# Optimization experiments

Measured on AMD Instinct MI355X. Metric: run time of the kernel, lower is better.

## Reference

```python
import jax, jax.numpy as jnp
import numpy as np

N = 100000
E = 1600000
F_IN = 64
F_OUT = 64
C = 1.0
MIN_NORM = 1e-15
BALL_EPS = 4e-3  # float32 eps in HGCN PoincareBall.proj


def _norm(x):
    return jnp.clip(jnp.linalg.norm(x, axis=-1, keepdims=True), MIN_NORM)


def artanh(x):
    return jnp.arctanh(jnp.clip(x, -1.0 + 1e-7, 1.0 - 1e-7))


def proj(x, c):
    # project back onto the Poincare ball of curvature -c
    norm = _norm(x)
    maxnorm = (1.0 - BALL_EPS) / jnp.sqrt(c)
    return jnp.where(norm > maxnorm, x / norm * maxnorm, x)


def mobius_matvec(m, x, c):
    sqrt_c = jnp.sqrt(c)
    x_norm = _norm(x)
    mx = x @ m.T
    mx_norm = _norm(mx)
    res = jnp.tanh(mx_norm / x_norm * artanh(sqrt_c * x_norm)) * mx / (mx_norm * sqrt_c)
    zero_mx = jnp.all(mx == 0, axis=-1, keepdims=True)
    return jnp.where(zero_mx, jnp.zeros_like(res), res)


def expmap0(u, c):
    sqrt_c = jnp.sqrt(c)
    u_norm = _norm(u)
    return jnp.tanh(sqrt_c * u_norm) * u / (sqrt_c * u_norm)


def mobius_add(x, y, c):
    x2 = jnp.sum(x * x, axis=-1, keepdims=True)
    y2 = jnp.sum(y * y, axis=-1, keepdims=True)
    xy = jnp.sum(x * y, axis=-1, keepdims=True)
    num = (1.0 + 2.0 * c * xy + c * y2) * x + (1.0 - c * x2) * y
    denom = 1.0 + 2.0 * c * xy + c * c * x2 * y2
    return num / jnp.clip(denom, MIN_NORM)


def hyp_linear(x, W, b, c):
    res = proj(mobius_matvec(W, x, c), c)
    if b is not None:
        hyp_bias = proj(expmap0(b[None, :], c), c)
        res = proj(mobius_add(res, hyp_bias, c), c)
    return res


def scatter_mean(edge_index, x, n):
    # mean of source features over edges landing at each target node; 0 if isolated
    src, dst = edge_index[0], edge_index[1]
    s = jax.ops.segment_sum(x[src], dst, num_segments=n)
    cnt = jax.ops.segment_sum(jnp.ones((src.shape[0], 1), x.dtype), dst, num_segments=n)
    return s / jnp.clip(cnt, 1.0)


def setup_inputs() -> dict:
    key = jax.random.key(0)
    ks = jax.random.split(key, 9)
    glorot = 1.0 / np.sqrt(F_IN)
    return {
        "x": jax.random.normal(ks[0], (N, F_IN), dtype=jnp.float32) * 0.1,
        "W_pos": jax.random.uniform(ks[1], (F_OUT, F_IN), jnp.float32, -glorot, glorot),
        "W_pos_cc": jax.random.uniform(ks[2], (F_OUT, F_IN), jnp.float32, -glorot, glorot),
        "b_pos_cc": jax.random.uniform(ks[3], (F_OUT,), jnp.float32, -glorot, glorot),
        "W_neg": jax.random.uniform(ks[4], (F_OUT, F_IN), jnp.float32, -glorot, glorot),
        "W_neg_cc": jax.random.uniform(ks[5], (F_OUT, F_IN), jnp.float32, -glorot, glorot),
        "b_neg_cc": jax.random.uniform(ks[6], (F_OUT,), jnp.float32, -glorot, glorot),
        "pos_edge_index": jax.random.randint(ks[7], (2, E), 0, N, dtype=jnp.int64) if jax.config.jax_enable_x64 else jax.random.randint(ks[7], (2, E), 0, N, dtype=jnp.int32),
        "neg_edge_index": jax.random.randint(ks[8], (2, E), 0, N, dtype=jnp.int32),
    }


def reference(x, W_pos, W_pos_cc, b_pos_cc, W_neg, W_neg_cc, b_neg_cc, pos_edge_index, neg_edge_index):
    n = x.shape[0]
    # first_aggr=True branch of HSignedConv.forward
    agg_pos = scatter_mean(pos_edge_index, x, n)          # [N, F_IN]
    out_pos = hyp_linear(agg_pos, W_pos, None, C)
    out_pos = out_pos + hyp_linear(x, W_pos_cc, b_pos_cc, C)
    agg_neg = scatter_mean(neg_edge_index, x, n)
    out_neg = hyp_linear(agg_neg, W_neg, None, C)
    out_neg = out_neg + hyp_linear(x, W_neg_cc, b_neg_cc, C)
    return jnp.concatenate([out_pos, out_neg], axis=-1)  # [N, 2*F_OUT]
```

## Files before the change

### kernel.cpp

```cpp
#include <hip/hip_runtime.h>
#include <math.h>

#define NN 100000
#define BSZ 256
#define NB 391
#define NB2 782
constexpr float MAXNORM_C = 0.996f;
constexpr float MINNORM_C = 1e-15f;

__global__ void prep_transpose(const float* __restrict__ Wp, const float* __restrict__ Wpc,
                               const float* __restrict__ Wn, const float* __restrict__ Wnc,
                               float* __restrict__ wt) {
    int idx = blockIdx.x * 256 + threadIdx.x;
    int m = idx >> 12;
    int k = (idx >> 6) & 63;
    int j = idx & 63;
    const float* W = (m == 0) ? Wp : (m == 1) ? Wpc : (m == 2) ? Wn : Wnc;
    wt[idx] = W[j * 64 + k];
}

__device__ inline float wave_sum64(float v) {
    #pragma unroll
    for (int m = 32; m >= 1; m >>= 1) v += __shfl_xor(v, m, 64);
    return v;
}

__global__ void prep_bias(const float* __restrict__ bp, const float* __restrict__ bn,
                          float* __restrict__ hb) {
    int l = threadIdx.x;
    #pragma unroll
    for (int h = 0; h < 2; ++h) {
        float u = (h ? bn : bp)[l];
        float norm = fmaxf(sqrtf(wave_sum64(u * u)), MINNORM_C);
        float s = tanhf(norm) / norm;
        float v = s * u;
        float vn = fmaxf(sqrtf(wave_sum64(v * v)), MINNORM_C);
        if (vn > MAXNORM_C) v *= MAXNORM_C / vn;
        float y2 = wave_sum64(v * v);
        hb[h * 65 + l] = v;
        if (l == 0) hb[h * 65 + 64] = y2;
    }
}

__global__ __launch_bounds__(256) void bucket_count(
    const int* __restrict__ pei, int E1,
    const int* __restrict__ nei, int E2,
    int* __restrict__ gcnt) {
    __shared__ int h[NB2];
    int tid = threadIdx.x;
    for (int i = tid; i < NB2; i += 256) h[i] = 0;
    __syncthreads();
    int tot = E1 + E2;
    int base = blockIdx.x * 8192;
    #pragma unroll 4
    for (int k = 0; k < 32; ++k) {
        int idx = base + k * 256 + tid;
        if (idx < tot) {
            int half = idx >= E1;
            int e = idx - (half ? E1 : 0);
            const int* ei = half ? nei : pei;
            int E = half ? E2 : E1;
            int dst = ei[E + e];
            atomicAdd(&h[half * NB + (dst >> 8)], 1);
        }
    }
    __syncthreads();
    for (int i = tid; i < NB2; i += 256) {
        int c = h[i];
        if (c) atomicAdd(&gcnt[i], c);
    }
}

__global__ void bucket_scan(const int* __restrict__ gcnt, int* __restrict__ goffs,
                            int* __restrict__ gcursor) {
    __shared__ int tmp[256];
    int tid = threadIdx.x;
    int base = tid * 4;
    int items[4];
    int s = 0;
    #pragma unroll
    for (int i = 0; i < 4; ++i) {
        items[i] = (base + i < NB2) ? gcnt[base + i] : 0;
        s += items[i];
    }
    tmp[tid] = s;
    __syncthreads();
    for (int off = 1; off < 256; off <<= 1) {
        int v = (tid >= off) ? tmp[tid - off] : 0;
        __syncthreads();
        tmp[tid] += v;
        __syncthreads();
    }
    int run = tmp[tid] - s;
    #pragma unroll
    for (int i = 0; i < 4; ++i) {
        if (base + i < NB2) { goffs[base + i] = run; gcursor[base + i] = run; }
        run += items[i];
    }
}

__global__ __launch_bounds__(256) void bucket_scatter(
    const int* __restrict__ pei, int E1,
    const int* __restrict__ nei, int E2,
    int* __restrict__ gcursor, int* __restrict__ packed) {
    __shared__ int h[NB2];
    __shared__ int hb[NB2];
    int tid = threadIdx.x;
    for (int i = tid; i < NB2; i += 256) h[i] = 0;
    __syncthreads();
    int tot = E1 + E2;
    int base = blockIdx.x * 8192;
    #pragma unroll 4
    for (int k = 0; k < 32; ++k) {
        int idx = base + k * 256 + tid;
        if (idx < tot) {
            int half = idx >= E1;
            int e = idx - (half ? E1 : 0);
            const int* ei = half ? nei : pei;
            int E = half ? E2 : E1;
            int dst = ei[E + e];
            atomicAdd(&h[half * NB + (dst >> 8)], 1);
        }
    }
    __syncthreads();
    for (int i = tid; i < NB2; i += 256) {
        int c = h[i];
        hb[i] = c ? atomicAdd(&gcursor[i], c) : 0;
    }
    __syncthreads();
    for (int i = tid; i < NB2; i += 256) h[i] = 0;
    __syncthreads();
    #pragma unroll 4
    for (int k = 0; k < 32; ++k) {
        int idx = base + k * 256 + tid;
        if (idx < tot) {
            int half = idx >= E1;
            int e = idx - (half ? E1 : 0);
            const int* ei = half ? nei : pei;
            int E = half ? E2 : E1;
            int src = ei[e];
            int dst = ei[E + e];
            int b = half * NB + (dst >> 8);
            int r = atomicAdd(&h[b], 1);
            packed[hb[b] + r] = (src << 8) | (dst & 255);
        }
    }
}

__global__ __launch_bounds__(256) void node_sort(
    const int* __restrict__ goffs, const int* __restrict__ gcnt,
    const int* __restrict__ packed,
    int* __restrict__ esrc, int* __restrict__ ndeg, int* __restrict__ noffs) {
    __shared__ int h[256];
    __shared__ int sc[256];
    int tid = threadIdx.x;
    int bucket = blockIdx.x;
    int start = goffs[bucket];
    int cnt = gcnt[bucket];
    h[tid] = 0;
    __syncthreads();
    for (int i = start + tid; i < start + cnt; i += 256)
        atomicAdd(&h[packed[i] & 255], 1);
    __syncthreads();
    int deg = h[tid];
    sc[tid] = deg;
    __syncthreads();
    for (int off = 1; off < 256; off <<= 1) {
        int v = (tid >= off) ? sc[tid - off] : 0;
        __syncthreads();
        sc[tid] += v;
        __syncthreads();
    }
    int excl = sc[tid] - deg;
    int half = bucket >= NB;
    int node = (bucket - (half ? NB : 0)) * BSZ + tid;
    if (node < NN) {
        ndeg[half * NN + node] = deg;
        noffs[half * NN + node] = start + excl;
    }
    h[tid] = excl;
    __syncthreads();
    for (int i = start + tid; i < start + cnt; i += 256) {
        int p = packed[i];
        int r = atomicAdd(&h[p & 255], 1);
        esrc[start + r] = p >> 8;
    }
}

__global__ __launch_bounds__(256) void gather_kernel(
    const int* __restrict__ noffs, const int* __restrict__ ndeg,
    const int* __restrict__ esrc, const float* __restrict__ x,
    float* __restrict__ out) {
    int wid = (blockIdx.x * 256 + threadIdx.x) >> 6;
    int lane = threadIdx.x & 63;
    if (wid >= 2 * NN) return;
    int half = wid >= NN;
    int node = wid - (half ? NN : 0);
    int start = noffs[wid];
    int deg = ndeg[wid];
    float acc = 0.f;
    for (int b = 0; b < deg; b += 64) {
        int n = min(64, deg - b);
        int s_l = (b + lane < deg) ? esrc[start + b + lane] : 0;
        int i = 0;
        for (; i + 4 <= n; i += 4) {
            int a0 = __shfl(s_l, i, 64), a1 = __shfl(s_l, i + 1, 64);
            int a2 = __shfl(s_l, i + 2, 64), a3 = __shfl(s_l, i + 3, 64);
            float v0 = x[a0 * 64 + lane], v1 = x[a1 * 64 + lane];
            float v2 = x[a2 * 64 + lane], v3 = x[a3 * 64 + lane];
            acc += (v0 + v1) + (v2 + v3);
        }
        for (; i < n; ++i) acc += x[__shfl(s_l, i, 64) * 64 + lane];
    }
    float m = acc / fmaxf((float)deg, 1.f);
    out[(size_t)node * 128 + half * 64 + lane] = m;
}

__device__ __attribute__((always_inline)) inline void hyp_mm_proj(
        const float* vp, const float* __restrict__ wtm, float (&mx)[64]) {
    #pragma unroll
    for (int j = 0; j < 64; ++j) mx[j] = 0.f;
    float vn2 = 0.f;
    for (int k0 = 0; k0 < 64; k0 += 4) {
        float4 a4 = *(const float4*)(vp + k0);
        float a0 = a4.x, a1 = a4.y, a2 = a4.z, a3 = a4.w;
        vn2 = fmaf(a0, a0, fmaf(a1, a1, fmaf(a2, a2, fmaf(a3, a3, vn2))));
        const float* w0 = wtm + k0 * 64;
        #pragma unroll
        for (int j = 0; j < 64; ++j) {
            float m = mx[j];
            m = fmaf(a0, w0[j],        m);
            m = fmaf(a1, w0[64 + j],   m);
            m = fmaf(a2, w0[128 + j],  m);
            m = fmaf(a3, w0[192 + j],  m);
            mx[j] = m;
        }
    }
    float mn2 = 0.f;
    #pragma unroll
    for (int j = 0; j < 64; ++j) mn2 = fmaf(mx[j], mx[j], mn2);
    float xnorm = fmaxf(sqrtf(vn2), MINNORM_C);
    float mnorm = fmaxf(sqrtf(mn2), MINNORM_C);
    float z = fminf(xnorm, 1.0f - 1e-7f);
    float art = 0.5f * logf((1.0f + z) / (1.0f - z));
    float t = tanhf(mnorm / xnorm * art);
    float scale = (mn2 == 0.f) ? 0.f : (t / mnorm);
    #pragma unroll
    for (int j = 0; j < 64; ++j) mx[j] *= scale;
    float rn2 = 0.f;
    #pragma unroll
    for (int j = 0; j < 64; ++j) rn2 = fmaf(mx[j], mx[j], rn2);
    float rnorm = fmaxf(sqrtf(rn2), MINNORM_C);
    float f = (rnorm > MAXNORM_C) ? (MAXNORM_C / rnorm) : 1.0f;
    #pragma unroll
    for (int j = 0; j < 64; ++j) mx[j] *= f;
}

__global__ __launch_bounds__(256, 2) void finalize_kernel(
    const float* __restrict__ x,
    const float* __restrict__ wt,
    const float* __restrict__ hb,
    float* __restrict__ out) {
    int half = blockIdx.x & 1;
    int group = (blockIdx.x >> 1) * 4 + (threadIdx.x >> 6);
    int lane = threadIdx.x & 63;
    int node = group * 64 + lane;
    bool valid = node < NN;
    int nc = valid ? node : NN - 1;
    float* op = out + (size_t)nc * 128 + half * 64;

    const float* wtA = wt + half * 8192;
    const float* wtB = wtA + 4096;
    const float* hbh = hb + half * 65;

    float resA[64];
    hyp_mm_proj(op, wtA, resA);

    float resB[64];
    hyp_mm_proj(x + (size_t)nc * 64, wtB, resB);

    float x2 = 0.f, xy = 0.f;
    #pragma unroll
    for (int j = 0; j < 64; ++j) {
        x2 = fmaf(resB[j], resB[j], x2);
        xy = fmaf(resB[j], hbh[j], xy);
    }
    float y2 = hbh[64];
    float A = 1.f + 2.f * xy + y2;
    float B = 1.f - x2;
    float den = 1.f + 2.f * xy + x2 * y2;
    float dinv = 1.f / fmaxf(den, MINNORM_C);
    float rn2 = 0.f;
    #pragma unroll
    for (int j = 0; j < 64; ++j) {
        float r = (A * resB[j] + B * hbh[j]) * dinv;
        resB[j] = r;
        rn2 = fmaf(r, r, rn2);
    }
    float rnorm = fmaxf(sqrtf(rn2), MINNORM_C);
    float f = (rnorm > MAXNORM_C) ? (MAXNORM_C / rnorm) : 1.0f;

    if (valid) {
        #pragma unroll
        for (int k0 = 0; k0 < 64; k0 += 4) {
            float4 s;
            s.x = resA[k0 + 0] + resB[k0 + 0] * f;
            s.y = resA[k0 + 1] + resB[k0 + 1] * f;
            s.z = resA[k0 + 2] + resB[k0 + 2] * f;
            s.w = resA[k0 + 3] + resB[k0 + 3] * f;
            *(float4*)(op + k0) = s;
        }
    }
}

extern "C" void kernel_launch(void* const* d_in, const int* in_sizes, int n_in,
                              void* d_out, int out_size, void* d_ws, size_t ws_size,
                              hipStream_t stream) {
    const float* x   = (const float*)d_in[0];
    const float* Wp  = (const float*)d_in[1];
    const float* Wpc = (const float*)d_in[2];
    const float* bp  = (const float*)d_in[3];
    const float* Wn  = (const float*)d_in[4];
    const float* Wnc = (const float*)d_in[5];
    const float* bn  = (const float*)d_in[6];
    const int* pei = (const int*)d_in[7];
    const int* nei = (const int*)d_in[8];
    float* out = (float*)d_out;

    int E1 = in_sizes[7] / 2;
    int E2 = in_sizes[8] / 2;
    int tot = E1 + E2;

    int*   gcnt    = (int*)d_ws;
    int*   goffs   = gcnt + NB2;
    int*   gcursor = goffs + NB2;
    int*   ndeg    = gcursor + NB2 + 2;
    int*   noffs   = ndeg + 2 * NN;
    float* hbp     = (float*)(noffs + 2 * NN);
    float* wt      = hbp + 192;
    int*   packed  = (int*)(wt + 16384);
    int*   esrc    = packed + tot;

    hipMemsetAsync(gcnt, 0, NB2 * sizeof(int), stream);

    prep_transpose<<<64, 256, 0, stream>>>(Wp, Wpc, Wn, Wnc, wt);
    prep_bias<<<1, 64, 0, stream>>>(bp, bn, hbp);

    int nblk = (tot + 8191) / 8192;
    bucket_count<<<nblk, 256, 0, stream>>>(pei, E1, nei, E2, gcnt);
    bucket_scan<<<1, 256, 0, stream>>>(gcnt, goffs, gcursor);
    bucket_scatter<<<nblk, 256, 0, stream>>>(pei, E1, nei, E2, gcursor, packed);
    node_sort<<<NB2, 256, 0, stream>>>(goffs, gcnt, packed, esrc, ndeg, noffs);

    gather_kernel<<<(2 * NN * 64 + 255) / 256, 256, 0, stream>>>(noffs, ndeg, esrc, x, out);

    int groups = (NN + 63) / 64;
    int blocks = 2 * ((groups + 3) / 4);
    finalize_kernel<<<blocks, 256, 0, stream>>>(x, wt, hbp, out);
}
```

Before: 463.6 us.

## Split per-node hyperbolic matvec across 16 lanes with quad-packed weights

The finalize kernel now gives each node to 16 lanes instead of one thread. Each lane computes 4 output features from a weight layout repacked for float4 loads, and the norms are combined with cross-lane shuffle reductions. The change removes the 64-element per-thread register arrays, which means far less register pressure and higher occupancy. The redundant recomputation of the post-scale norm is replaced by algebra (scale^2 * mn2). In exchange, each lane reads the full input row and adds several shuffle reductions per node, and the grid assumes NN is divisible by 16.

```diff
diff --git a/kernel.cpp b/kernel.cpp
--- a/kernel.cpp
+++ b/kernel.cpp
@@ -8,20 +8,30 @@
 constexpr float MAXNORM_C = 0.996f;
 constexpr float MINNORM_C = 1e-15f;
 
-__global__ void prep_transpose(const float* __restrict__ Wp, const float* __restrict__ Wpc,
-                               const float* __restrict__ Wn, const float* __restrict__ Wnc,
-                               float* __restrict__ wt) {
+__global__ void prep_quad(const float* __restrict__ Wp, const float* __restrict__ Wpc,
+                          const float* __restrict__ Wn, const float* __restrict__ Wnc,
+                          float* __restrict__ wq) {
     int idx = blockIdx.x * 256 + threadIdx.x;
-    int m = idx >> 12;
-    int k = (idx >> 6) & 63;
-    int j = idx & 63;
+    int c  = idx & 3;
+    int r  = (idx >> 2) & 3;
+    int li = (idx >> 4) & 15;
+    int kg = (idx >> 8) & 15;
+    int m  = idx >> 12;
     const float* W = (m == 0) ? Wp : (m == 1) ? Wpc : (m == 2) ? Wn : Wnc;
-    wt[idx] = W[j * 64 + k];
+    wq[idx] = W[(li * 4 + r) * 64 + kg * 4 + c];
 }
 
 __device__ inline float wave_sum64(float v) {
     #pragma unroll
     for (int m = 32; m >= 1; m >>= 1) v += __shfl_xor(v, m, 64);
+    return v;
+}
+
+__device__ inline float qreduce(float v) {
+    v += __shfl_xor(v, 1, 64);
+    v += __shfl_xor(v, 2, 64);
+    v += __shfl_xor(v, 4, 64);
+    v += __shfl_xor(v, 8, 64);
     return v;
 }
 
@@ -216,101 +226,84 @@
     out[(size_t)node * 128 + half * 64 + lane] = m;
 }
 
-__device__ __attribute__((always_inline)) inline void hyp_mm_proj(
-        const float* vp, const float* __restrict__ wtm, float (&mx)[64]) {
-    #pragma unroll
-    for (int j = 0; j < 64; ++j) mx[j] = 0.f;
+__device__ __attribute__((always_inline)) inline float4 quad_hyp(
+        const float* __restrict__ vrow, const float* __restrict__ wq, int li) {
+    float a0 = 0.f, a1 = 0.f, a2 = 0.f, a3 = 0.f;
     float vn2 = 0.f;
-    for (int k0 = 0; k0 < 64; k0 += 4) {
-        float4 a4 = *(const float4*)(vp + k0);
-        float a0 = a4.x, a1 = a4.y, a2 = a4.z, a3 = a4.w;
-        vn2 = fmaf(a0, a0, fmaf(a1, a1, fmaf(a2, a2, fmaf(a3, a3, vn2))));
-        const float* w0 = wtm + k0 * 64;
-        #pragma unroll
-        for (int j = 0; j < 64; ++j) {
-            float m = mx[j];
-            m = fmaf(a0, w0[j],        m);
-            m = fmaf(a1, w0[64 + j],   m);
-            m = fmaf(a2, w0[128 + j],  m);
-            m = fmaf(a3, w0[192 + j],  m);
-            mx[j] = m;
-        }
-    }
-    float mn2 = 0.f;
-    #pragma unroll
-    for (int j = 0; j < 64; ++j) mn2 = fmaf(mx[j], mx[j], mn2);
+    #pragma unroll
+    for (int kg = 0; kg < 16; ++kg) {
+        float4 v4 = *(const float4*)(vrow + kg * 4);
+        vn2 = fmaf(v4.x, v4.x, fmaf(v4.y, v4.y, fmaf(v4.z, v4.z, fmaf(v4.w, v4.w, vn2))));
+        const float* wb = wq + (kg * 16 + li) * 16;
+        float4 w0 = *(const float4*)(wb);
+        float4 w1 = *(const float4*)(wb + 4);
+        float4 w2 = *(const float4*)(wb + 8);
+        float4 w3 = *(const float4*)(wb + 12);
+        a0 = fmaf(w0.x, v4.x, fmaf(w0.y, v4.y, fmaf(w0.z, v4.z, fmaf(w0.w, v4.w, a0))));
+        a1 = fmaf(w1.x, v4.x, fmaf(w1.y, v4.y, fmaf(w1.z, v4.z, fmaf(w1.w, v4.w, a1))));
+        a2 = fmaf(w2.x, v4.x, fmaf(w2.y, v4.y, fmaf(w2.z, v4.z, fmaf(w2.w, v4.w, a2))));
+        a3 = fmaf(w3.x, v4.x, fmaf(w3.y, v4.y, fmaf(w3.z, v4.z, fmaf(w3.w, v4.w, a3))));
+    }
+    float mn2 = qreduce(fmaf(a0, a0, fmaf(a1, a1, fmaf(a2, a2, a3 * a3))));
     float xnorm = fmaxf(sqrtf(vn2), MINNORM_C);
     float mnorm = fmaxf(sqrtf(mn2), MINNORM_C);
     float z = fminf(xnorm, 1.0f - 1e-7f);
     float art = 0.5f * logf((1.0f + z) / (1.0f - z));
     float t = tanhf(mnorm / xnorm * art);
     float scale = (mn2 == 0.f) ? 0.f : (t / mnorm);
-    #pragma unroll
-    for (int j = 0; j < 64; ++j) mx[j] *= scale;
-    float rn2 = 0.f;
-    #pragma unroll
-    for (int j = 0; j < 64; ++j) rn2 = fmaf(mx[j], mx[j], rn2);
+    float rn2 = scale * scale * mn2;
     float rnorm = fmaxf(sqrtf(rn2), MINNORM_C);
     float f = (rnorm > MAXNORM_C) ? (MAXNORM_C / rnorm) : 1.0f;
-    #pragma unroll
-    for (int j = 0; j < 64; ++j) mx[j] *= f;
-}
-
-__global__ __launch_bounds__(256, 2) void finalize_kernel(
+    float sf = scale * f;
+    return make_float4(a0 * sf, a1 * sf, a2 * sf, a3 * sf);
+}
+
+__global__ __launch_bounds__(256) void finalize_kernel(
     const float* __restrict__ x,
-    const float* __restrict__ wt,
+    const float* __restrict__ wq,
     const float* __restrict__ hb,
     float* __restrict__ out) {
     int half = blockIdx.x & 1;
-    int group = (blockIdx.x >> 1) * 4 + (threadIdx.x >> 6);
+    int nb = blockIdx.x >> 1;
+    int wave = threadIdx.x >> 6;
     int lane = threadIdx.x & 63;
-    int node = group * 64 + lane;
-    bool valid = node < NN;
-    int nc = valid ? node : NN - 1;
-    float* op = out + (size_t)nc * 128 + half * 64;
-
-    const float* wtA = wt + half * 8192;
-    const float* wtB = wtA + 4096;
+    int g = lane >> 4;
+    int li = lane & 15;
+    int node = nb * 16 + wave * 4 + g;
+
+    const float* wqA = wq + (half * 2) * 4096;
+    const float* wqB = wqA + 4096;
     const float* hbh = hb + half * 65;
-
-    float resA[64];
-    hyp_mm_proj(op, wtA, resA);
-
-    float resB[64];
-    hyp_mm_proj(x + (size_t)nc * 64, wtB, resB);
-
-    float x2 = 0.f, xy = 0.f;
-    #pragma unroll
-    for (int j = 0; j < 64; ++j) {
-        x2 = fmaf(resB[j], resB[j], x2);
-        xy = fmaf(resB[j], hbh[j], xy);
-    }
+    float* op = out + (size_t)node * 128 + half * 64;
+
+    float4 resA = quad_hyp(op, wqA, li);
+
+    float4 resB = quad_hyp(x + (size_t)node * 64, wqB, li);
+
+    float4 h4 = *(const float4*)(hbh + li * 4);
+    float x2 = qreduce(fmaf(resB.x, resB.x, fmaf(resB.y, resB.y,
+                       fmaf(resB.z, resB.z, resB.w * resB.w))));
+    float xy = qreduce(fmaf(resB.x, h4.x, fmaf(resB.y, h4.y,
+                       fmaf(resB.z, h4.z, resB.w * h4.w))));
     float y2 = hbh[64];
     float A = 1.f + 2.f * xy + y2;
     float B = 1.f - x2;
     float den = 1.f + 2.f * xy + x2 * y2;
     float dinv = 1.f / fmaxf(den, MINNORM_C);
-    float rn2 = 0.f;
-    #pragma unroll
-    for (int j = 0; j < 64; ++j) {
-        float r = (A * resB[j] + B * hbh[j]) * dinv;
-        resB[j] = r;
-        rn2 = fmaf(r, r, rn2);
-    }
+    float r0 = (A * resB.x + B * h4.x) * dinv;
+    float r1 = (A * resB.y + B * h4.y) * dinv;
+    float r2 = (A * resB.z + B * h4.z) * dinv;
+    float r3 = (A * resB.w + B * h4.w) * dinv;
+    float rn2 = qreduce(fmaf(r0, r0, fmaf(r1, r1, fmaf(r2, r2, r3 * r3))));
     float rnorm = fmaxf(sqrtf(rn2), MINNORM_C);
     float f = (rnorm > MAXNORM_C) ? (MAXNORM_C / rnorm) : 1.0f;
 
-    if (valid) {
-        #pragma unroll
-        for (int k0 = 0; k0 < 64; k0 += 4) {
-            float4 s;
-            s.x = resA[k0 + 0] + resB[k0 + 0] * f;
-            s.y = resA[k0 + 1] + resB[k0 + 1] * f;
-            s.z = resA[k0 + 2] + resB[k0 + 2] * f;
-            s.w = resA[k0 + 3] + resB[k0 + 3] * f;
-            *(float4*)(op + k0) = s;
-        }
-    }
+    float4 s;
+    s.x = resA.x + r0 * f;
+    s.y = resA.y + r1 * f;
+    s.z = resA.z + r2 * f;
+    s.w = resA.w + r3 * f;
+    *(float4*)(op + li * 4) = s;
 }
 
 extern "C" void kernel_launch(void* const* d_in, const int* in_sizes, int n_in,
@@ -337,13 +330,13 @@
     int*   ndeg    = gcursor + NB2 + 2;
     int*   noffs   = ndeg + 2 * NN;
     float* hbp     = (float*)(noffs + 2 * NN);
-    float* wt      = hbp + 192;
-    int*   packed  = (int*)(wt + 16384);
+    float* wq      = hbp + 192;
+    int*   packed  = (int*)(wq + 16384);
     int*   esrc    = packed + tot;
 
     hipMemsetAsync(gcnt, 0, NB2 * sizeof(int), stream);
 
-    prep_transpose<<<64, 256, 0, stream>>>(Wp, Wpc, Wn, Wnc, wt);
+    prep_quad<<<64, 256, 0, stream>>>(Wp, Wpc, Wn, Wnc, wq);
     prep_bias<<<1, 64, 0, stream>>>(bp, bn, hbp);
 
     int nblk = (tot + 8191) / 8192;
@@ -354,7 +347,5 @@
 
     gather_kernel<<<(2 * NN * 64 + 255) / 256, 256, 0, stream>>>(noffs, ndeg, esrc, x, out);
 
-    int groups = (NN + 63) / 64;
-    int blocks = 2 * ((groups + 3) / 4);
-    finalize_kernel<<<blocks, 256, 0, stream>>>(x, wt, hbp, out);
-}
+    finalize_kernel<<<2 * (NN / 16), 256, 0, stream>>>(x, wq, hbp, out);
+}
```

After: 706.0 us. 1.52x slower.
